# Kernel tuning notes

Hardware: AMD Instinct MI355X
Metric: run time of the kernel (lower is better)

Reference implementation:

```python
import jax, jax.numpy as jnp
import numpy as np
from jax import lax

B, N, C, H, W = 1024, 32, 3, 5, 5
NUM_ACTIONS = 16
OBS_IN = 34           # 2 pos + N one-hot
OBS_ACT_IN = 50       # OBS_IN + NUM_ACTIONS
D_EMB = 128
OBS_OUT = 128
OBS_ACT_OUT = 128     # forced by mask_attn_values width 128
FINAL_IN = 256
FINAL_OUT = 16

def leaky(x):
    return jnp.where(x > 0, x, 0.01 * x)

def _lin(x, w, b):
    # torch Linear: y = x @ W^T + b, W: [out, in]
    return x @ w.T + b

def setup_inputs() -> dict:
    key = jax.random.key(0)
    ks = jax.random.split(key, 24)
    f32 = jnp.float32
    inp = {}
    inp['agent_states'] = jax.random.normal(ks[0], (B, N, C, H, W), f32)
    inp['agent_global_positions'] = jax.random.uniform(ks[1], (B, N, 2), f32)
    # real one-hot agent ids, same for every batch element
    inp['agent_one_hot_encoding'] = jnp.broadcast_to(jnp.eye(N, dtype=f32), (B, N, N))
    inp['policies'] = jax.random.uniform(ks[2], (B, N, NUM_ACTIONS), f32)
    inp['actions'] = jax.random.uniform(ks[3], (B, N, NUM_ACTIONS), f32)
    s = 0.05
    inp['conv1_w'] = jax.random.normal(ks[4], (16, C, 3, 3), f32) * s
    inp['conv1_b'] = jnp.zeros((16,), f32)
    inp['conv2_w'] = jax.random.normal(ks[5], (32, 16, 3, 3), f32) * s
    inp['conv2_b'] = jnp.zeros((32,), f32)
    inp['sa_w'] = jax.random.normal(ks[6], (D_EMB, 32 + OBS_ACT_IN), f32) * s
    inp['sa_b'] = jnp.zeros((D_EMB,), f32)
    inp['s_w'] = jax.random.normal(ks[7], (D_EMB, 32 + OBS_IN), f32) * s
    inp['s_b'] = jnp.zeros((D_EMB,), f32)
    inp['k_w'] = jax.random.normal(ks[8], (OBS_ACT_OUT, D_EMB), f32) * s
    inp['k_b'] = jnp.zeros((OBS_ACT_OUT,), f32)
    inp['q_w'] = jax.random.normal(ks[9], (OBS_OUT, D_EMB), f32) * s
    inp['q_b'] = jnp.zeros((OBS_OUT,), f32)
    inp['v_w'] = jax.random.normal(ks[10], (OBS_ACT_OUT, D_EMB), f32) * s
    inp['v_b'] = jnp.zeros((OBS_ACT_OUT,), f32)
    inp['sq_w'] = jax.random.normal(ks[11], (OBS_OUT, 32 + OBS_IN), f32) * s
    inp['sq_b'] = jnp.zeros((OBS_OUT,), f32)
    inp['f1_w'] = jax.random.normal(ks[12], (64, FINAL_IN), f32) * s
    inp['f1_b'] = jnp.zeros((64,), f32)
    inp['f2_w'] = jax.random.normal(ks[13], (FINAL_OUT, 64), f32) * s
    inp['f2_b'] = jnp.zeros((FINAL_OUT,), f32)
    return inp

# off-diagonal gather indices: row i -> all j != i, in increasing order
_OFFDIAG = np.stack([np.delete(np.arange(N), i) for i in range(N)])  # [N, N-1]

def reference(agent_states, agent_global_positions, agent_one_hot_encoding,
              policies, actions,
              conv1_w, conv1_b, conv2_w, conv2_b,
              sa_w, sa_b, s_w, s_b, k_w, k_b, q_w, q_b, v_w, v_b,
              sq_w, sq_b, f1_w, f1_b, f2_w, f2_b):
    b, n = agent_states.shape[0], agent_states.shape[1]
    pose = jnp.concatenate([agent_global_positions, agent_one_hot_encoding], axis=-1)
    x = agent_states.reshape(-1, agent_states.shape[-3], agent_states.shape[-2], agent_states.shape[-1])
    dn = ('NCHW', 'OIHW', 'NCHW')
    x = leaky(lax.conv_general_dilated(x, conv1_w, (1, 1), 'VALID', dimension_numbers=dn) + conv1_b[None, :, None, None])
    x = leaky(lax.conv_general_dilated(x, conv2_w, (1, 1), 'VALID', dimension_numbers=dn) + conv2_b[None, :, None, None])
    states = jnp.concatenate([x.reshape(b, n, -1), pose], axis=-1)        # [B,N,32+OBS_IN]
    state_actions = jnp.concatenate([states, actions], axis=-1)           # [B,N,32+OBS_ACT_IN]
    se = leaky(_lin(states, s_w, s_b))                                    # [B,N,128]
    sa = leaky(_lin(state_actions, sa_w, sa_b))                           # [B,N,128]
    keys = _lin(sa, k_w, k_b)
    queries = _lin(se, q_w, q_b)
    score = jnp.einsum('bnd,bmd->bnm', queries, keys) / jnp.sqrt(jnp.float32(OBS_ACT_OUT))
    idx = jnp.asarray(_OFFDIAG)
    score_off = jnp.take_along_axis(score, idx[None], axis=-1)            # [B,N,N-1] self-excluded
    weight = jax.nn.softmax(score_off, axis=-1)
    vals = _lin(sa, v_w, v_b)                                             # [B,N,128]
    vals_off = vals[:, idx, :]                                            # [B,N,N-1,128]
    agg = jnp.einsum('bnmk,bnm->bnk', vals_off, weight)                   # weighted sum over others
    sq = leaky(_lin(states, sq_w, sq_b))
    node = jnp.concatenate([sq, agg], axis=-1)                            # [B,N,256]
    value = _lin(leaky(_lin(node, f1_w, f1_b)), f2_w, f2_b)               # [B,N,FINAL_OUT]
    return value, weight
```

## Files before the change

kernel.cpp:

```cpp
#include <hip/hip_runtime.h>
#include <hip/hip_bf16.h>

typedef unsigned int u32;
typedef unsigned short u16;
typedef __attribute__((ext_vector_type(8))) short short8;
typedef __attribute__((ext_vector_type(4))) float f32x4;

#define DEVI __device__ __forceinline__

DEVI float asf(u32 u){ union{u32 i; float f;} v; v.i=u; return v.f; }
DEVI u16 f2b(float x){ u32 b = __float_as_uint(x); u32 r = b + 0x7fffu + ((b>>16)&1u); return (u16)(r>>16); }
DEVI float b2f(u16 h){ return asf(((u32)h)<<16); }
DEVI float lk(float x){ return x > 0.f ? x : 0.01f*x; }
DEVI short8 lds8(const u16* p){ return *reinterpret_cast<const short8*>(p); }

#define MFMA(a,b,c) __builtin_amdgcn_mfma_f32_16x16x32_bf16((a),(b),(c),0,0,0)

#define FRAG_P4_OFF 36864
#define FRAG_P8_OFF 86016
#define FRAG_P9_OFF 102400
#define FRAG_TOTAL  103424

__global__ void prelude_k(const float* __restrict__ sw, const float* __restrict__ saw,
                          const float* __restrict__ sqw,
                          const float* __restrict__ qw, const float* __restrict__ kw,
                          const float* __restrict__ vw,
                          const float* __restrict__ f1w, const float* __restrict__ f2w,
                          u16* __restrict__ frag)
{
    int idx = blockIdx.x*256 + threadIdx.x;
    if (idx >= FRAG_TOTAL) return;
    if (idx < FRAG_P4_OFF) {
        int j = idx & 7, lane = (idx>>3)&63, r2 = idx>>9;
        int ks = r2 % 3, nt = r2 / 3;
        int fl = lane&15, kg = lane>>4;
        int k = ks*32 + kg*8 + j;
        float w = 0.f;
        if (nt < 8)       { int c = nt*16+fl;      if (k < 66) w = sw[c*66+k]; }
        else if (nt < 16) { int c = (nt-8)*16+fl;  if (k < 82) w = saw[c*82+k]; }
        else              { int c = (nt-16)*16+fl; if (k < 66) w = sqw[c*66+k]; }
        frag[idx] = f2b(w);
    } else if (idx < FRAG_P8_OFF) {
        int e = idx - FRAG_P4_OFF;
        int j = e&7, lane = (e>>3)&63, r2 = e>>9;
        int ks = r2 & 3, nt = r2 >> 2;
        int fl = lane&15, kg = lane>>4;
        int k = ks*32 + kg*8 + j;
        float w;
        if (nt < 8)       w = qw[(nt*16+fl)*128 + k];
        else if (nt < 16) w = kw[((nt-8)*16+fl)*128 + k];
        else              w = vw[((nt-16)*16+fl)*128 + k];
        frag[idx] = f2b(w);
    } else if (idx < FRAG_P9_OFF) {
        int e = idx - FRAG_P8_OFF;
        int j = e&7, lane = (e>>3)&63, r2 = e>>9;
        int ks = r2&7, nt = r2>>3;
        int k = ks*32 + (lane>>4)*8 + j;
        frag[idx] = f2b(f1w[(nt*16+(lane&15))*256 + k]);
    } else {
        int e = idx - FRAG_P9_OFF;
        int j = e&7, lane = (e>>3)&63, r2 = e>>9;
        int k = r2*32 + (lane>>4)*8 + j;
        frag[idx] = f2b(f2w[(lane&15)*64 + k]);
    }
}

#define L_STH 0
#define L_QH  0
#define L_SQH 8704
#define L_IM  8704
#define L_SEH 17408
#define L_SCF 17408
#define L_H1  17408
#define L_SAH 26112
#define L_W32 26112
#define L_C1H 31744
#define L_KH  34816
#define L_AGG 34816
#define L_FC2 42496
#define L_VT  43520
#define SMEM_BYTES 53760

__global__ __launch_bounds__(512, 6)
void fused_kernel(const float* __restrict__ xs, const float* __restrict__ pos,
                  const float* __restrict__ oh, const float* __restrict__ act,
                  const float* __restrict__ c1w, const float* __restrict__ c1b,
                  const float* __restrict__ c2w, const float* __restrict__ c2b,
                  const float* __restrict__ sb,  const float* __restrict__ sab,
                  const float* __restrict__ sqb,
                  const float* __restrict__ qb,  const float* __restrict__ kb,
                  const float* __restrict__ vb,
                  const float* __restrict__ f1b, const float* __restrict__ f2b_,
                  float* __restrict__ outv, float* __restrict__ outw,
                  const u16* __restrict__ frag)
{
    __shared__ __align__(16) char smem[SMEM_BYTES];

    const int b = blockIdx.x, tid = threadIdx.x;
    const int lane = tid & 63, wv = tid >> 6;
    const int fl = lane & 15, kg = lane >> 4;

    u16* STh = (u16*)(smem + L_STH);
    u16* SQh = (u16*)(smem + L_SQH);
    u16* SEh = (u16*)(smem + L_SEH);
    u16* SAh = (u16*)(smem + L_SAH);
    u16* Qh  = (u16*)(smem + L_QH);
    u16* Kh  = (u16*)(smem + L_KH);
    u16* Vt  = (u16*)(smem + L_VT);
    u16* IM   = (u16*)(smem + L_IM);
    u16* C1h  = (u16*)(smem + L_C1H);
    u16* FC2L = (u16*)(smem + L_FC2);
    float* SCf = (float*)(smem + L_SCF);
    u16* W32h = (u16*)(smem + L_W32);
    u16* AGGh = (u16*)(smem + L_AGG);
    u16* H1h  = (u16*)(smem + L_H1);
    const u16* F3  = frag;
    const u16* F4  = frag + FRAG_P4_OFF;
    const u16* F8  = frag + FRAG_P8_OFF;
    const u16* F9  = frag + FRAG_P9_OFF;

    for (int i = tid; i < 64; i += 512)   { int n=i>>1, j=i&1;  STh[n*136+32+j] = f2b(pos[(b*32+n)*2+j]); }
    for (int i = tid; i < 1024; i += 512) { int n=i>>5, m=i&31; STh[n*136+34+m] = f2b(oh[(b*32+n)*32+m]); }
    { int n=tid>>4, j=tid&15; STh[n*136+66+j] = f2b(act[(b*32+n)*16+j]); }
    for (int i = tid; i < 448; i += 512)  { int n=i/14, j=i-n*14; STh[n*136+82+j] = 0; }
    {
        int j = tid & 7, l2 = tid >> 3;
        int k = (l2 >> 4)*8 + j;
        IM[l2*40 + 32 + j] = f2b((k < 27) ? c1w[(l2 & 15)*27 + k] : 0.f);
    }
    for (int e = tid; e < 5120; e += 512) {
        int j = e & 7, l2 = (e >> 3) & 63, r2 = e >> 9;
        int ks = r2 % 5, nt = r2 / 5;
        int k = ks*32 + (l2 >> 4)*8 + j;
        FC2L[e] = f2b((k < 144) ? c2w[(nt*16 + (l2 & 15))*144 + k] : 0.f);
    }
    {
        const float* xp = xs + b*2400;
        for (int e = tid; e < 9216; e += 512) {
            int row = e >> 5, k = e & 31;
            int n = row / 9, p = row - n*9;
            float v = 0.f;
            if (k < 27) {
                int ic = k / 9, q = k - ic*9;
                int y = p/3 + q/3, x = (p - (p/3)*3) + (q - (q/3)*3);
                v = xp[n*75 + ic*25 + y*5 + x];
            }
            IM[row*40 + k] = f2b(v);
        }
    }
    for (int i = tid; i < 768; i += 512) { int n = i/24, j = i - n*24; C1h[n*168 + 144 + j] = 0; }
    __syncthreads();

    for (int t = wv; t < 18; t += 8) {
        f32x4 acc = {0.f,0.f,0.f,0.f};
        acc = MFMA(lds8(IM + (t*16 + fl)*40 + kg*8), lds8(IM + lane*40 + 32), acc);
        float bv = c1b[fl];
        #pragma unroll
        for (int r = 0; r < 4; ++r) {
            int row = t*16 + kg*4 + r;
            int n = row / 9, p = row - n*9;
            C1h[n*168 + fl*9 + p] = f2b(lk(acc[r] + bv));
        }
    }
    __syncthreads();

    if (wv < 4) {
        int mt = wv >> 1, nt = wv & 1;
        f32x4 acc = {0.f,0.f,0.f,0.f};
        const u16* ap = C1h + (mt*16 + fl)*168 + kg*8;
        const u16* bp = FC2L + ((nt*5)*64 + lane)*8;
        #pragma unroll
        for (int ks = 0; ks < 5; ++ks)
            acc = MFMA(lds8(ap + ks*32), lds8(bp + ks*512), acc);
        float bv = c2b[nt*16 + fl];
        #pragma unroll
        for (int r = 0; r < 4; ++r)
            STh[(mt*16 + kg*4 + r)*136 + nt*16 + fl] = f2b(lk(acc[r] + bv));
    }
    __syncthreads();

    for (int t = wv; t < 48; t += 8) {
        int nt = t >> 1, mt = t & 1;
        f32x4 acc = {0.f,0.f,0.f,0.f};
        const u16* ap = STh + (mt*16 + fl)*136 + kg*8;
        const u16* bp = F3 + ((nt*3)*64 + lane)*8;
        #pragma unroll
        for (int ks = 0; ks < 3; ++ks)
            acc = MFMA(lds8(ap + ks*32), lds8(bp + ks*512), acc);
        u16* dst; const float* bias; int colOff;
        if (nt < 8)       { dst = SEh; bias = sb;  colOff = nt*16; }
        else if (nt < 16) { dst = SAh; bias = sab; colOff = (nt-8)*16; }
        else              { dst = SQh; bias = sqb; colOff = (nt-16)*16; }
        float bv = bias[colOff + fl];
        int rowb = mt*16 + kg*4;
        #pragma unroll
        for (int r = 0; r < 4; ++r)
            dst[(rowb+r)*136 + colOff + fl] = f2b(lk(acc[r] + bv));
    }
    __syncthreads();

    for (int t = wv; t < 48; t += 8) {
        int nt = t >> 1, mt = t & 1;
        const u16* A = (nt < 8) ? SEh : SAh;
        f32x4 acc = {0.f,0.f,0.f,0.f};
        const u16* ap = A + (mt*16 + fl)*136 + kg*8;
        const u16* bp = F4 + ((nt*4)*64 + lane)*8;
        #pragma unroll
        for (int ks = 0; ks < 4; ++ks)
            acc = MFMA(lds8(ap + ks*32), lds8(bp + ks*512), acc);
        int rowb = mt*16 + kg*4;
        if (nt < 8) {
            float bv = qb[nt*16 + fl];
            #pragma unroll
            for (int r = 0; r < 4; ++r)
                Qh[(rowb+r)*136 + nt*16 + fl] = f2b((acc[r] + bv)*0.08838834764831845f);
        } else if (nt < 16) {
            float bv = kb[(nt-8)*16 + fl];
            #pragma unroll
            for (int r = 0; r < 4; ++r)
                Kh[(rowb+r)*136 + (nt-8)*16 + fl] = f2b(acc[r] + bv);
        } else {
            int c = (nt-16)*16 + fl;
            float bv = vb[c];
            #pragma unroll
            for (int r = 0; r < 4; ++r)
                Vt[c*40 + rowb + r] = f2b(acc[r] + bv);
        }
    }
    __syncthreads();

    if (wv < 4) {
        int nt = wv >> 1, mt = wv & 1;
        f32x4 acc = {0.f,0.f,0.f,0.f};
        const u16* ap = Qh + (mt*16 + fl)*136 + kg*8;
        const u16* bp = Kh + (nt*16 + fl)*136 + kg*8;
        #pragma unroll
        for (int ks = 0; ks < 4; ++ks)
            acc = MFMA(lds8(ap + ks*32), lds8(bp + ks*32), acc);
        int rowb = mt*16 + kg*4;
        #pragma unroll
        for (int r = 0; r < 4; ++r)
            SCf[(rowb+r)*36 + nt*16 + fl] = acc[r];
    }
    __syncthreads();

    {
        int n = tid >> 4, g = tid & 15;
        int m0 = (g < n) ? g : g+1;
        int j1 = g + 16;
        bool v1 = j1 < 31;
        int m1 = (j1 < n) ? j1 : j1+1;
        float e0 = SCf[n*36 + m0];
        float e1 = v1 ? SCf[n*36 + m1] : -1e30f;
        float mx = fmaxf(e0, e1);
        #pragma unroll
        for (int d = 8; d; d >>= 1) mx = fmaxf(mx, __shfl_xor(mx, d, 16));
        float x0 = __expf(e0 - mx);
        float x1 = v1 ? __expf(e1 - mx) : 0.f;
        float s = x0 + x1;
        #pragma unroll
        for (int d = 8; d; d >>= 1) s += __shfl_xor(s, d, 16);
        float inv = 1.f/s;
        float w0 = x0*inv, w1 = x1*inv;
        W32h[n*40 + m0] = f2b(w0);
        if (v1) W32h[n*40 + m1] = f2b(w1);
        if (g == 0) W32h[n*40 + n] = 0;
        float* wp = outw + (b*32 + n)*31;
        wp[g] = w0;
        if (v1) wp[j1] = w1;
    }
    __syncthreads();

    for (int t = wv; t < 16; t += 8) {
        int nt = t >> 1, mt = t & 1;
        f32x4 acc = {0.f,0.f,0.f,0.f};
        acc = MFMA(lds8(W32h + (mt*16 + fl)*40 + kg*8),
                   lds8(Vt + (nt*16 + fl)*40 + kg*8), acc);
        int rowb = mt*16 + kg*4;
        #pragma unroll
        for (int r = 0; r < 4; ++r)
            AGGh[(rowb+r)*136 + nt*16 + fl] = f2b(acc[r]);
    }
    __syncthreads();

    {
        int t = wv;
        int nt = t >> 1, mt = t & 1;
        f32x4 acc = {0.f,0.f,0.f,0.f};
        const u16* bp = F8 + ((nt*8)*64 + lane)*8;
        #pragma unroll
        for (int ks = 0; ks < 8; ++ks) {
            const u16* ap = ((ks < 4) ? SQh : AGGh) + (mt*16 + fl)*136 + (ks&3)*32 + kg*8;
            acc = MFMA(lds8(ap), lds8(bp + ks*512), acc);
        }
        float bv = f1b[nt*16 + fl];
        int rowb = mt*16 + kg*4;
        #pragma unroll
        for (int r = 0; r < 4; ++r)
            H1h[(rowb+r)*72 + nt*16 + fl] = f2b(lk(acc[r] + bv));
    }
    __syncthreads();

    if (wv < 2) {
        int mt = wv;
        f32x4 acc = {0.f,0.f,0.f,0.f};
        const u16* ap = H1h + (mt*16 + fl)*72 + kg*8;
        const u16* bp = F9 + lane*8;
        #pragma unroll
        for (int ks = 0; ks < 2; ++ks)
            acc = MFMA(lds8(ap + ks*32), lds8(bp + ks*512), acc);
        float bv = f2b_[fl];
        int rowb = mt*16 + kg*4;
        #pragma unroll
        for (int r = 0; r < 4; ++r)
            outv[(b*32 + rowb + r)*16 + fl] = acc[r] + bv;
    }
}

extern "C" void kernel_launch(void* const* d_in, const int* in_sizes, int n_in,
                              void* d_out, int out_size, void* d_ws, size_t ws_size,
                              hipStream_t stream) {
    const int B = in_sizes[0] / (32*75);
    u16* frag = (u16*)d_ws;

    const int PRE_GRID = (FRAG_TOTAL + 255)/256;
    prelude_k<<<PRE_GRID, 256, 0, stream>>>(
        (const float*)d_in[11], (const float*)d_in[9],  (const float*)d_in[19],
        (const float*)d_in[15], (const float*)d_in[13], (const float*)d_in[17],
        (const float*)d_in[21], (const float*)d_in[23], frag);

    fused_kernel<<<B, 512, 0, stream>>>(
        (const float*)d_in[0],  (const float*)d_in[1],  (const float*)d_in[2],
        (const float*)d_in[4],
        (const float*)d_in[5],  (const float*)d_in[6],
        (const float*)d_in[7],  (const float*)d_in[8],
        (const float*)d_in[12], (const float*)d_in[10], (const float*)d_in[20],
        (const float*)d_in[16], (const float*)d_in[14], (const float*)d_in[18],
        (const float*)d_in[22], (const float*)d_in[24],
        (float*)d_out, (float*)d_out + (size_t)B*32*16, frag);
}
```

Baseline: 154.3 us.

## Prefetch weight fragments into registers and fuse score with softmax

Each wave now loads its global weight fragments for the projection, Q/K/V and f1 GEMMs into registers before the preceding barrier. The next tile's B fragments are software-pipelined during the MFMA loops, and each wave keeps its A fragment resident while it iterates over column tiles. The QK^T score computation is fused with the masked softmax in registers, which removes the fp32 score buffer in LDS and one barrier. Launch bounds are relaxed to 4 waves per SIMD to leave room for the extra live registers, at the cost of possibly lower occupancy.

```diff
diff --git a/kernel.cpp b/kernel.cpp
--- a/kernel.cpp
+++ b/kernel.cpp
@@ -10,7 +10,6 @@
 
 DEVI float asf(u32 u){ union{u32 i; float f;} v; v.i=u; return v.f; }
 DEVI u16 f2b(float x){ u32 b = __float_as_uint(x); u32 r = b + 0x7fffu + ((b>>16)&1u); return (u16)(r>>16); }
-DEVI float b2f(u16 h){ return asf(((u32)h)<<16); }
 DEVI float lk(float x){ return x > 0.f ? x : 0.01f*x; }
 DEVI short8 lds8(const u16* p){ return *reinterpret_cast<const short8*>(p); }
 
@@ -70,7 +69,6 @@
 #define L_SQH 8704
 #define L_IM  8704
 #define L_SEH 17408
-#define L_SCF 17408
 #define L_H1  17408
 #define L_SAH 26112
 #define L_W32 26112
@@ -81,7 +79,7 @@
 #define L_VT  43520
 #define SMEM_BYTES 53760
 
-__global__ __launch_bounds__(512, 6)
+__global__ __launch_bounds__(512, 4)
 void fused_kernel(const float* __restrict__ xs, const float* __restrict__ pos,
                   const float* __restrict__ oh, const float* __restrict__ act,
                   const float* __restrict__ c1w, const float* __restrict__ c1b,
@@ -99,6 +97,7 @@
     const int b = blockIdx.x, tid = threadIdx.x;
     const int lane = tid & 63, wv = tid >> 6;
     const int fl = lane & 15, kg = lane >> 4;
+    const int mt = wv & 1, nb = wv >> 1;
 
     u16* STh = (u16*)(smem + L_STH);
     u16* SQh = (u16*)(smem + L_SQH);
@@ -110,7 +109,6 @@
     u16* IM   = (u16*)(smem + L_IM);
     u16* C1h  = (u16*)(smem + L_C1H);
     u16* FC2L = (u16*)(smem + L_FC2);
-    float* SCf = (float*)(smem + L_SCF);
     u16* W32h = (u16*)(smem + L_W32);
     u16* AGGh = (u16*)(smem + L_AGG);
     u16* H1h  = (u16*)(smem + L_H1);
@@ -136,7 +134,9 @@
     }
     {
         const float* xp = xs + b*2400;
-        for (int e = tid; e < 9216; e += 512) {
+        #pragma unroll
+        for (int i = 0; i < 18; ++i) {
+            int e = tid + i*512;
             int row = e >> 5, k = e & 31;
             int n = row / 9, p = row - n*9;
             float v = 0.f;
@@ -151,132 +151,161 @@
     for (int i = tid; i < 768; i += 512) { int n = i/24, j = i - n*24; C1h[n*168 + 144 + j] = 0; }
     __syncthreads();
 
-    for (int t = wv; t < 18; t += 8) {
+    {
+        short8 bw = lds8(IM + lane*40 + 32);
+        for (int t = wv; t < 18; t += 8) {
+            f32x4 acc = {0.f,0.f,0.f,0.f};
+            acc = MFMA(lds8(IM + (t*16 + fl)*40 + kg*8), bw, acc);
+            float bv = c1b[fl];
+            #pragma unroll
+            for (int r = 0; r < 4; ++r) {
+                int row = t*16 + kg*4 + r;
+                int n = row / 9, p = row - n*9;
+                C1h[n*168 + fl*9 + p] = f2b(lk(acc[r] + bv));
+            }
+        }
+    }
+    __syncthreads();
+
+    if (wv < 4) {
+        int m2 = wv >> 1, n2 = wv & 1;
         f32x4 acc = {0.f,0.f,0.f,0.f};
-        acc = MFMA(lds8(IM + (t*16 + fl)*40 + kg*8), lds8(IM + lane*40 + 32), acc);
-        float bv = c1b[fl];
-        #pragma unroll
-        for (int r = 0; r < 4; ++r) {
-            int row = t*16 + kg*4 + r;
-            int n = row / 9, p = row - n*9;
-            C1h[n*168 + fl*9 + p] = f2b(lk(acc[r] + bv));
-        }
-    }
-    __syncthreads();
-
-    if (wv < 4) {
-        int mt = wv >> 1, nt = wv & 1;
-        f32x4 acc = {0.f,0.f,0.f,0.f};
-        const u16* ap = C1h + (mt*16 + fl)*168 + kg*8;
-        const u16* bp = FC2L + ((nt*5)*64 + lane)*8;
+        const u16* ap = C1h + (m2*16 + fl)*168 + kg*8;
+        const u16* bp = FC2L + ((n2*5)*64 + lane)*8;
         #pragma unroll
         for (int ks = 0; ks < 5; ++ks)
             acc = MFMA(lds8(ap + ks*32), lds8(bp + ks*512), acc);
-        float bv = c2b[nt*16 + fl];
+        float bv = c2b[n2*16 + fl];
         #pragma unroll
         for (int r = 0; r < 4; ++r)
-            STh[(mt*16 + kg*4 + r)*136 + nt*16 + fl] = f2b(lk(acc[r] + bv));
-    }
-    __syncthreads();
-
-    for (int t = wv; t < 48; t += 8) {
-        int nt = t >> 1, mt = t & 1;
-        f32x4 acc = {0.f,0.f,0.f,0.f};
+            STh[(m2*16 + kg*4 + r)*136 + n2*16 + fl] = f2b(lk(acc[r] + bv));
+    }
+    short8 pb0, pb1, pb2;
+    {
+        const short8* p = (const short8*)(F3 + ((nb*3)*64 + lane)*8);
+        pb0 = p[0]; pb1 = p[64]; pb2 = p[128];
+    }
+    __syncthreads();
+
+    {
         const u16* ap = STh + (mt*16 + fl)*136 + kg*8;
-        const u16* bp = F3 + ((nt*3)*64 + lane)*8;
-        #pragma unroll
-        for (int ks = 0; ks < 3; ++ks)
-            acc = MFMA(lds8(ap + ks*32), lds8(bp + ks*512), acc);
-        u16* dst; const float* bias; int colOff;
-        if (nt < 8)       { dst = SEh; bias = sb;  colOff = nt*16; }
-        else if (nt < 16) { dst = SAh; bias = sab; colOff = (nt-8)*16; }
-        else              { dst = SQh; bias = sqb; colOff = (nt-16)*16; }
-        float bv = bias[colOff + fl];
-        int rowb = mt*16 + kg*4;
-        #pragma unroll
-        for (int r = 0; r < 4; ++r)
-            dst[(rowb+r)*136 + colOff + fl] = f2b(lk(acc[r] + bv));
-    }
-    __syncthreads();
-
-    for (int t = wv; t < 48; t += 8) {
-        int nt = t >> 1, mt = t & 1;
-        const u16* A = (nt < 8) ? SEh : SAh;
-        f32x4 acc = {0.f,0.f,0.f,0.f};
-        const u16* ap = A + (mt*16 + fl)*136 + kg*8;
-        const u16* bp = F4 + ((nt*4)*64 + lane)*8;
-        #pragma unroll
-        for (int ks = 0; ks < 4; ++ks)
-            acc = MFMA(lds8(ap + ks*32), lds8(bp + ks*512), acc);
-        int rowb = mt*16 + kg*4;
-        if (nt < 8) {
-            float bv = qb[nt*16 + fl];
+        short8 a0 = lds8(ap), a1 = lds8(ap+32), a2 = lds8(ap+64);
+        short8 b0 = pb0, b1 = pb1, b2 = pb2;
+        #pragma unroll
+        for (int k = 0; k < 6; ++k) {
+            const int nt = nb + 4*k;
+            short8 c0 = b0, c1 = b1, c2 = b2;
+            if (k < 5) {
+                const short8* p = (const short8*)(F3 + (((nb + 4*(k+1))*3)*64 + lane)*8);
+                b0 = p[0]; b1 = p[64]; b2 = p[128];
+            }
+            f32x4 acc = {0.f,0.f,0.f,0.f};
+            acc = MFMA(a0, c0, acc); acc = MFMA(a1, c1, acc); acc = MFMA(a2, c2, acc);
+            u16* dst; const float* bias; int colOff;
+            if (nt < 8)       { dst = SEh; bias = sb;  colOff = nt*16; }
+            else if (nt < 16) { dst = SAh; bias = sab; colOff = (nt-8)*16; }
+            else              { dst = SQh; bias = sqb; colOff = (nt-16)*16; }
+            float bv = bias[colOff + fl];
+            int rowb = mt*16 + kg*4;
             #pragma unroll
             for (int r = 0; r < 4; ++r)
-                Qh[(rowb+r)*136 + nt*16 + fl] = f2b((acc[r] + bv)*0.08838834764831845f);
-        } else if (nt < 16) {
-            float bv = kb[(nt-8)*16 + fl];
+                dst[(rowb+r)*136 + colOff + fl] = f2b(lk(acc[r] + bv));
+        }
+    }
+    short8 qb0, qb1, qb2, qb3;
+    {
+        const short8* p = (const short8*)(F4 + ((nb*4)*64 + lane)*8);
+        qb0 = p[0]; qb1 = p[64]; qb2 = p[128]; qb3 = p[192];
+    }
+    __syncthreads();
+
+    {
+        const u16* apSE = SEh + (mt*16 + fl)*136 + kg*8;
+        short8 a0 = lds8(apSE), a1 = lds8(apSE+32), a2 = lds8(apSE+64), a3 = lds8(apSE+96);
+        short8 b0 = qb0, b1 = qb1, b2 = qb2, b3 = qb3;
+        #pragma unroll
+        for (int k = 0; k < 6; ++k) {
+            const int nt = nb + 4*k;
+            if (k == 2) {
+                const u16* apSA = SAh + (mt*16 + fl)*136 + kg*8;
+                a0 = lds8(apSA); a1 = lds8(apSA+32); a2 = lds8(apSA+64); a3 = lds8(apSA+96);
+            }
+            short8 c0 = b0, c1 = b1, c2 = b2, c3 = b3;
+            if (k < 5) {
+                const short8* p = (const short8*)(F4 + (((nb + 4*(k+1))*4)*64 + lane)*8);
+                b0 = p[0]; b1 = p[64]; b2 = p[128]; b3 = p[192];
+            }
+            f32x4 acc = {0.f,0.f,0.f,0.f};
+            acc = MFMA(a0, c0, acc); acc = MFMA(a1, c1, acc);
+            acc = MFMA(a2, c2, acc); acc = MFMA(a3, c3, acc);
+            int rowb = mt*16 + kg*4;
+            if (nt < 8) {
+                float bv = qb[nt*16 + fl];
+                #pragma unroll
+                for (int r = 0; r < 4; ++r)
+                    Qh[(rowb+r)*136 + nt*16 + fl] = f2b((acc[r] + bv)*0.08838834764831845f);
+            } else if (nt < 16) {
+                float bv = kb[(nt-8)*16 + fl];
+                #pragma unroll
+                for (int r = 0; r < 4; ++r)
+                    Kh[(rowb+r)*136 + (nt-8)*16 + fl] = f2b(acc[r] + bv);
+            } else {
+                int c = (nt-16)*16 + fl;
+                float bv = vb[c];
+                #pragma unroll
+                for (int r = 0; r < 4; ++r)
+                    Vt[c*40 + rowb + r] = f2b(acc[r] + bv);
+            }
+        }
+    }
+    __syncthreads();
+
+    if (wv < 2) {
+        const u16* ap = Qh + (wv*16 + fl)*136 + kg*8;
+        short8 a0 = lds8(ap), a1 = lds8(ap+32), a2 = lds8(ap+64), a3 = lds8(ap+96);
+        const u16* bp0 = Kh + fl*136 + kg*8;
+        const u16* bp1 = Kh + (16 + fl)*136 + kg*8;
+        f32x4 acc0 = {0.f,0.f,0.f,0.f}, acc1 = {0.f,0.f,0.f,0.f};
+        acc0 = MFMA(a0, lds8(bp0), acc0);     acc0 = MFMA(a1, lds8(bp0+32), acc0);
+        acc0 = MFMA(a2, lds8(bp0+64), acc0);  acc0 = MFMA(a3, lds8(bp0+96), acc0);
+        acc1 = MFMA(a0, lds8(bp1), acc1);     acc1 = MFMA(a1, lds8(bp1+32), acc1);
+        acc1 = MFMA(a2, lds8(bp1+64), acc1);  acc1 = MFMA(a3, lds8(bp1+96), acc1);
+        #pragma unroll
+        for (int r = 0; r < 4; ++r) {
+            const int n = wv*16 + kg*4 + r;
+            const int m0 = fl, m1 = fl + 16;
+            float e0 = (m0 == n) ? -3e38f : acc0[r];
+            float e1 = (m1 == n) ? -3e38f : acc1[r];
+            float mx = fmaxf(e0, e1);
             #pragma unroll
-            for (int r = 0; r < 4; ++r)
-                Kh[(rowb+r)*136 + (nt-8)*16 + fl] = f2b(acc[r] + bv);
-        } else {
-            int c = (nt-16)*16 + fl;
-            float bv = vb[c];
+            for (int d = 8; d; d >>= 1) mx = fmaxf(mx, __shfl_xor(mx, d, 16));
+            float x0 = (m0 == n) ? 0.f : __expf(e0 - mx);
+            float x1 = (m1 == n) ? 0.f : __expf(e1 - mx);
+            float s = x0 + x1;
             #pragma unroll
-            for (int r = 0; r < 4; ++r)
-                Vt[c*40 + rowb + r] = f2b(acc[r] + bv);
-        }
-    }
-    __syncthreads();
-
-    if (wv < 4) {
-        int nt = wv >> 1, mt = wv & 1;
+            for (int d = 8; d; d >>= 1) s += __shfl_xor(s, d, 16);
+            float inv = 1.f/s;
+            float w0 = x0*inv, w1 = x1*inv;
+            W32h[n*40 + m0] = f2b(w0);
+            W32h[n*40 + m1] = f2b(w1);
+            float* wp = outw + (b*32 + n)*31;
+            if (m0 != n) wp[(m0 < n) ? m0 : m0-1] = w0;
+            if (m1 != n) wp[(m1 < n) ? m1 : m1-1] = w1;
+        }
+    }
+    __syncthreads();
+
+    short8 f80,f81,f82,f83,f84,f85,f86,f87;
+    {
+        const short8* p = (const short8*)(F8 + ((nb*8)*64 + lane)*8);
+        f80=p[0]; f81=p[64]; f82=p[128]; f83=p[192]; f84=p[256]; f85=p[320]; f86=p[384]; f87=p[448];
+    }
+    for (int t = wv; t < 16; t += 8) {
+        int nt = t >> 1, m7 = t & 1;
         f32x4 acc = {0.f,0.f,0.f,0.f};
-        const u16* ap = Qh + (mt*16 + fl)*136 + kg*8;
-        const u16* bp = Kh + (nt*16 + fl)*136 + kg*8;
-        #pragma unroll
-        for (int ks = 0; ks < 4; ++ks)
-            acc = MFMA(lds8(ap + ks*32), lds8(bp + ks*32), acc);
-        int rowb = mt*16 + kg*4;
-        #pragma unroll
-        for (int r = 0; r < 4; ++r)
-            SCf[(rowb+r)*36 + nt*16 + fl] = acc[r];
-    }
-    __syncthreads();
-
-    {
-        int n = tid >> 4, g = tid & 15;
-        int m0 = (g < n) ? g : g+1;
-        int j1 = g + 16;
-        bool v1 = j1 < 31;
-        int m1 = (j1 < n) ? j1 : j1+1;
-        float e0 = SCf[n*36 + m0];
-        float e1 = v1 ? SCf[n*36 + m1] : -1e30f;
-        float mx = fmaxf(e0, e1);
-        #pragma unroll
-        for (int d = 8; d; d >>= 1) mx = fmaxf(mx, __shfl_xor(mx, d, 16));
-        float x0 = __expf(e0 - mx);
-        float x1 = v1 ? __expf(e1 - mx) : 0.f;
-        float s = x0 + x1;
-        #pragma unroll
-        for (int d = 8; d; d >>= 1) s += __shfl_xor(s, d, 16);
-        float inv = 1.f/s;
-        float w0 = x0*inv, w1 = x1*inv;
-        W32h[n*40 + m0] = f2b(w0);
-        if (v1) W32h[n*40 + m1] = f2b(w1);
-        if (g == 0) W32h[n*40 + n] = 0;
-        float* wp = outw + (b*32 + n)*31;
-        wp[g] = w0;
-        if (v1) wp[j1] = w1;
-    }
-    __syncthreads();
-
-    for (int t = wv; t < 16; t += 8) {
-        int nt = t >> 1, mt = t & 1;
-        f32x4 acc = {0.f,0.f,0.f,0.f};
-        acc = MFMA(lds8(W32h + (mt*16 + fl)*40 + kg*8),
+        acc = MFMA(lds8(W32h + (m7*16 + fl)*40 + kg*8),
                    lds8(Vt + (nt*16 + fl)*40 + kg*8), acc);
-        int rowb = mt*16 + kg*4;
+        int rowb = m7*16 + kg*4;
         #pragma unroll
         for (int r = 0; r < 4; ++r)
             AGGh[(rowb+r)*136 + nt*16 + fl] = f2b(acc[r]);
@@ -284,33 +313,37 @@
     __syncthreads();
 
     {
-        int t = wv;
-        int nt = t >> 1, mt = t & 1;
         f32x4 acc = {0.f,0.f,0.f,0.f};
-        const u16* bp = F8 + ((nt*8)*64 + lane)*8;
-        #pragma unroll
-        for (int ks = 0; ks < 8; ++ks) {
-            const u16* ap = ((ks < 4) ? SQh : AGGh) + (mt*16 + fl)*136 + (ks&3)*32 + kg*8;
-            acc = MFMA(lds8(ap), lds8(bp + ks*512), acc);
-        }
-        float bv = f1b[nt*16 + fl];
+        const u16* aq = SQh  + (mt*16 + fl)*136 + kg*8;
+        const u16* ag = AGGh + (mt*16 + fl)*136 + kg*8;
+        acc = MFMA(lds8(aq),      f80, acc);
+        acc = MFMA(lds8(aq+32),   f81, acc);
+        acc = MFMA(lds8(aq+64),   f82, acc);
+        acc = MFMA(lds8(aq+96),   f83, acc);
+        acc = MFMA(lds8(ag),      f84, acc);
+        acc = MFMA(lds8(ag+32),   f85, acc);
+        acc = MFMA(lds8(ag+64),   f86, acc);
+        acc = MFMA(lds8(ag+96),   f87, acc);
+        float bv = f1b[nb*16 + fl];
         int rowb = mt*16 + kg*4;
         #pragma unroll
         for (int r = 0; r < 4; ++r)
-            H1h[(rowb+r)*72 + nt*16 + fl] = f2b(lk(acc[r] + bv));
+            H1h[(rowb+r)*72 + nb*16 + fl] = f2b(lk(acc[r] + bv));
+    }
+    short8 b9a, b9b;
+    {
+        const short8* p = (const short8*)(F9 + lane*8);
+        b9a = p[0]; b9b = p[64];
     }
     __syncthreads();
 
     if (wv < 2) {
-        int mt = wv;
         f32x4 acc = {0.f,0.f,0.f,0.f};
-        const u16* ap = H1h + (mt*16 + fl)*72 + kg*8;
-        const u16* bp = F9 + lane*8;
-        #pragma unroll
-        for (int ks = 0; ks < 2; ++ks)
-            acc = MFMA(lds8(ap + ks*32), lds8(bp + ks*512), acc);
+        const u16* ap = H1h + (wv*16 + fl)*72 + kg*8;
+        acc = MFMA(lds8(ap), b9a, acc);
+        acc = MFMA(lds8(ap+32), b9b, acc);
         float bv = f2b_[fl];
-        int rowb = mt*16 + kg*4;
+        int rowb = wv*16 + kg*4;
         #pragma unroll
         for (int r = 0; r < 4; ++r)
             outv[(b*32 + rowb + r)*16 + fl] = acc[r] + bv;
```

Result: no change. 152.4 us (-1.3%).
